# Kernel optimization log

Measured on AMD Instinct MI355X. Metric: run time of the kernel, lower is better.

## Reference

```python
import jax, jax.numpy as jnp
import numpy as np

# graph/batch constants
B, N_PER, DEG, FEAT, K = 64, 1024, 16, 64, 10
N = B * N_PER            # 65536 total nodes
E = N * DEG              # 1048576 edges
HID = 2 * FEAT           # 128


def setup_inputs() -> dict:
    key = jax.random.key(0)
    ks = jax.random.split(key, 10)
    x = jax.random.normal(ks[0], (N, FEAT), jnp.float32)
    # intra-graph edges: local indices in [0, n) offset by graph id * n
    offs = (jnp.arange(B, dtype=jnp.int32) * N_PER)[:, None]
    edge_src = (jax.random.randint(ks[1], (B, N_PER * DEG), 0, N_PER, jnp.int32) + offs).reshape(-1)
    edge_dst = (jax.random.randint(ks[2], (B, N_PER * DEG), 0, N_PER, jnp.int32) + offs).reshape(-1)
    uniforms = jax.random.uniform(ks[3], (N, 3 * K), jnp.float32, 1e-6, 1.0 - 1e-6)

    def lin(k, i, o):
        s = 1.0 / np.sqrt(i)
        return jax.random.uniform(k, (i, o), jnp.float32, -s, s)

    return {
        "x": x, "edge_src": edge_src, "edge_dst": edge_dst, "uniforms": uniforms,
        "W0": lin(ks[4], FEAT, HID), "b0": jnp.zeros((HID,), jnp.float32),
        "W1": lin(ks[5], HID, HID), "b1": jnp.zeros((HID,), jnp.float32),
        "Wf": lin(ks[6], HID, HID), "bf": jnp.zeros((HID,), jnp.float32),
        "W2": lin(ks[7], 2 * HID, HID), "b2": jnp.zeros((HID,), jnp.float32),
        "W3": lin(ks[8], HID, 1), "b3": jnp.zeros((1,), jnp.float32),
    }


def _gcn_norm(src, dst):
    # GCNConv: add self-loops, symmetric deg^{-1/2} normalization
    loop = jnp.arange(N, dtype=src.dtype)
    s = jnp.concatenate([src, loop])
    d = jnp.concatenate([dst, loop])
    deg = jnp.zeros((N,), jnp.float32).at[d].add(1.0)
    dinv = jax.lax.rsqrt(deg)  # deg >= 1 because of self-loops
    return s, d, dinv[s] * dinv[d]


def _gcn(h, W, b, s, d, norm):
    h = h @ W                                                   # [N, out]
    agg = jnp.zeros((N, W.shape[1]), h.dtype).at[d].add(h[s] * norm[:, None])
    return agg + b


def reference(x, edge_src, edge_dst, uniforms, W0, b0, W1, b1, Wf, bf, W2, b2, W3, b3):
    s, d, norm = _gcn_norm(edge_src, edge_dst)
    # conv0 + global max pool + fc1 -> per-graph global info
    h0 = jax.nn.relu(_gcn(x, W0, b0, s, d, norm))               # [N, HID]
    glob = jnp.max(h0.reshape(B, N_PER, HID), axis=1) @ Wf + bf  # [B, HID]
    # two applications of the SAME conv1 (as in the source)
    h = jax.nn.relu(_gcn(h0, W1, b1, s, d, norm))
    h = jax.nn.relu(_gcn(h, W1, b1, s, d, norm))
    # ConcatenateLayer: [local, tiled global] per node (dropout is eval identity)
    h = jnp.concatenate([h, jnp.repeat(glob, N_PER, axis=0)], axis=-1)  # [N, 2*HID]
    h = jax.nn.relu(_gcn(h, W2, b2, s, d, norm))
    logits = _gcn(h, W3, b3, s, d, norm).reshape(B, N_PER)      # [B, n]
    # SampleConcrete (eval): per-graph top-k threshold mask
    th = jax.lax.top_k(logits, K)[0][:, -1]                     # kth-largest per graph
    mask = (logits >= th[:, None]).astype(jnp.float32)
    return mask.reshape(N, 1)
```

## Files before the change

kernel.cpp:

```cpp
#include <hip/hip_runtime.h>
#include <math.h>

#define NB    64
#define NPER  1024
#define NTOT  65536
#define ETOT  1048576
#define FEAT  64
#define HID   128
#define KSEL  10
#define MAXDEG 64


typedef __attribute__((ext_vector_type(8))) short bf16x8;
typedef __attribute__((ext_vector_type(4))) float f32x4;

static __device__ __forceinline__ unsigned short f2bf(float x) {
    unsigned u = __float_as_uint(x);
    return (unsigned short)((u + 0x7FFFu + ((u >> 16) & 1u)) >> 16);
}
static __device__ __forceinline__ float bf2f(unsigned short s) {
    return __uint_as_float(((unsigned)s) << 16);
}

__global__ __launch_bounds__(1024) void csrpack_k(const int* __restrict__ src,
                                                  const int* __restrict__ dst,
                                                  int* __restrict__ cnt,
                                                  unsigned short* __restrict__ col16,
                                                  const float* __restrict__ W0,
                                                  const float* __restrict__ W1,
                                                  const float* __restrict__ W2,
                                                  unsigned short* __restrict__ Wph,
                                                  unsigned short* __restrict__ Wpl,
                                                  float* __restrict__ part) {
    int t = threadIdx.x;
    int b = blockIdx.x;
    if (b >= NB) {
        int pb = b - NB;
        if (pb == 40) {
            for (int i = t; i < NB * 128; i += 1024) part[i] = 0.f;
            return;
        }
        int idx = pb * 1024 + t;
        if (idx >= 320 * 128) return;
        int k = idx >> 7;
        int c = idx & 127;
        float v;
        size_t mb;
        int kk;
        if (k < 64)       { kk = k;       v = W0[kk * 128 + c]; mb = 0; }
        else if (k < 192) { kk = k - 64;  v = W1[kk * 128 + c]; mb = (size_t)64 * 128; }
        else              { kk = k - 192; v = W2[kk * 128 + c]; mb = (size_t)192 * 128; }
        unsigned short h  = f2bf(v);
        unsigned short lo = f2bf(v - bf2f(h));
        size_t d = mb + ((size_t)(kk >> 3) * 128 + c) * 8 + (kk & 7);
        Wph[d] = h;
        Wpl[d] = lo;
        return;
    }
    __shared__ int lcnt[NPER];
    int g = b;
    int gbase = g << 10;
    int ebase = g * (NPER * 16);
    lcnt[t] = 0;
    __syncthreads();
    const int4* ds4 = (const int4*)(dst + ebase);
    const int4* ss4 = (const int4*)(src + ebase);
#pragma unroll 1
    for (int i = 0; i < 4; ++i) {
        int e4 = i * 1024 + t;
        int4 dv = ds4[e4];
        int4 sv = ss4[e4];
        int d0 = dv.x & (NPER - 1), s0 = sv.x & (NPER - 1);
        int d1 = dv.y & (NPER - 1), s1 = sv.y & (NPER - 1);
        int d2 = dv.z & (NPER - 1), s2 = sv.z & (NPER - 1);
        int d3 = dv.w & (NPER - 1), s3 = sv.w & (NPER - 1);
        int p0 = atomicAdd(&lcnt[d0], 1);
        col16[(size_t)(gbase + d0) * MAXDEG + p0] = (unsigned short)s0;
        int p1 = atomicAdd(&lcnt[d1], 1);
        col16[(size_t)(gbase + d1) * MAXDEG + p1] = (unsigned short)s1;
        int p2 = atomicAdd(&lcnt[d2], 1);
        col16[(size_t)(gbase + d2) * MAXDEG + p2] = (unsigned short)s2;
        int p3 = atomicAdd(&lcnt[d3], 1);
        col16[(size_t)(gbase + d3) * MAXDEG + p3] = (unsigned short)s3;
    }
    __syncthreads();
    cnt[gbase + t] = lcnt[t];
}

__global__ __launch_bounds__(1024) void agg_k(const float* __restrict__ Z,
                                              const float* __restrict__ x,
                                              const unsigned short* __restrict__ col16,
                                              const int* __restrict__ cnt,
                                              unsigned short* __restrict__ Ah,
                                              unsigned short* __restrict__ Al,
                                              int cshift,
                                              float* __restrict__ fvec,
                                              const float* __restrict__ Wf,
                                              const float* __restrict__ bfv,
                                              const float* __restrict__ W2g,
                                              float* __restrict__ gproj,
                                              const float* __restrict__ part) {
    __shared__ float4 sy4[4096];
    int t = threadIdx.x;

    if (Wf && (int)blockIdx.x >= (int)gridDim.x - NB) {
        float* sm = (float*)sy4;
        float* mp = sm;
        float* ps = sm + 128;
        float* gl = sm + 128 + 1024;
        int gg = blockIdx.x - (gridDim.x - NB);
        int o = t & 127, s8 = t >> 7;
        if (t < 128) mp[t] = part[(size_t)gg * 128 + t];
        __syncthreads();
        float p = 0.f;
#pragma unroll
        for (int q = 0; q < 16; ++q) { int k = s8 * 16 + q; p += mp[k] * Wf[(size_t)k * 128 + o]; }
        ps[t] = p;
        __syncthreads();
        if (t < 128) {
            float a = bfv[t];
#pragma unroll
            for (int q = 0; q < 8; ++q) a += ps[q * 128 + t];
            gl[t] = a;
        }
        __syncthreads();
        p = 0.f;
#pragma unroll
        for (int q = 0; q < 16; ++q) { int k = s8 * 16 + q; p += gl[k] * W2g[(size_t)(128 + k) * 128 + o]; }
        ps[t] = p;
        __syncthreads();
        if (t < 128) {
            float a = 0.f;
#pragma unroll
            for (int q = 0; q < 8; ++q) a += ps[q * 128 + t];
            gproj[(size_t)gg * 128 + t] = a;
        }
        return;
    }

    int g = blockIdx.x >> cshift;
    int c = blockIdx.x & ((1 << cshift) - 1);
    int gbase = g << 10;

    if (x) {
#pragma unroll
        for (int j = 0; j < 4; ++j) {
            int fl = j * 1024 + t;
            int v = fl >> 2, q = fl & 3;
            float dvv = rsqrtf((float)cnt[gbase + v] + 1.0f);
            float4 z = *(const float4*)&x[(size_t)(gbase + v) * FEAT + c * 16 + q * 4];
            z.x *= dvv; z.y *= dvv; z.z *= dvv; z.w *= dvv;
            sy4[fl] = z;
        }
    } else {
        const float4* Zg4 = (const float4*)(Z + ((size_t)c * NTOT + gbase) * 16);
#pragma unroll
        for (int j = 0; j < 4; ++j) sy4[j * 1024 + t] = Zg4[j * 1024 + t];
    }
    __syncthreads();

    int f4 = t & 3;
    int vl = t >> 2;

#pragma unroll 1
    for (int pass = 0; pass < 4; ++pass) {
        int v = pass * 256 + vl;
        int gv = gbase + v;
        int n = cnt[gv];
        float dv = rsqrtf((float)n + 1.0f);
        const unsigned short* ip = col16 + (size_t)gv * MAXDEG;
        float4 acc = sy4[v * 4 + f4];
        int i = 0;
        for (; i + 4 <= n; i += 4) {
            ushort4 s4 = *(const ushort4*)&ip[i];
            float4 y0 = sy4[(int)s4.x * 4 + f4];
            float4 y1 = sy4[(int)s4.y * 4 + f4];
            float4 y2 = sy4[(int)s4.z * 4 + f4];
            float4 y3 = sy4[(int)s4.w * 4 + f4];
            acc.x += (y0.x + y1.x) + (y2.x + y3.x);
            acc.y += (y0.y + y1.y) + (y2.y + y3.y);
            acc.z += (y0.z + y1.z) + (y2.z + y3.z);
            acc.w += (y0.w + y1.w) + (y2.w + y3.w);
        }
        for (; i < n; ++i) {
            float4 ya = sy4[(int)ip[i] * 4 + f4];
            acc.x += ya.x; acc.y += ya.y; acc.z += ya.z; acc.w += ya.w;
        }
        acc.x *= dv; acc.y *= dv; acc.z *= dv; acc.w *= dv;
        int krow = c * 16 + f4 * 4;
        size_t ba = ((size_t)(krow >> 3) * NTOT + gv) * 8 + (krow & 7);
        ushort4 h, lo;
        h.x = f2bf(acc.x); lo.x = f2bf(acc.x - bf2f(h.x));
        h.y = f2bf(acc.y); lo.y = f2bf(acc.y - bf2f(h.y));
        h.z = f2bf(acc.z); lo.z = f2bf(acc.z - bf2f(h.z));
        h.w = f2bf(acc.w); lo.w = f2bf(acc.w - bf2f(h.w));
        *(ushort4*)&Ah[ba] = h;
        *(ushort4*)&Al[ba] = lo;
    }

    if (fvec && c == 0) {
        __syncthreads();
        float* sdv = (float*)sy4;
        float dv = rsqrtf((float)cnt[gbase + t] + 1.0f);
        sdv[t] = dv;
        __syncthreads();
        int n = cnt[gbase + t];
        float acc = dv;
        const unsigned short* ip = col16 + (size_t)(gbase + t) * MAXDEG;
        int i = 0;
        for (; i + 4 <= n; i += 4) {
            ushort4 s4 = *(const ushort4*)&ip[i];
            acc += (sdv[s4.x] + sdv[s4.y]) + (sdv[s4.z] + sdv[s4.w]);
        }
        for (; i < n; ++i) acc += sdv[ip[i]];
        fvec[gbase + t] = dv * acc;
    }
}

__global__ __launch_bounds__(256, 4) void gemm_k(const unsigned short* __restrict__ Ah,
                                                 const unsigned short* __restrict__ Al,
                                                 const unsigned short* __restrict__ Wph,
                                                 const unsigned short* __restrict__ Wpl,
                                                 const float* __restrict__ bias,
                                                 float* __restrict__ outZ,
                                                 int K,
                                                 const float* __restrict__ fvec,
                                                 const float* __restrict__ gproj,
                                                 float* __restrict__ part,
                                                 const float* __restrict__ W3,
                                                 const int* __restrict__ cnt,
                                                 float* __restrict__ zout) {
    __shared__ __align__(16) unsigned short sAh[64 * 128];
    __shared__ __align__(16) unsigned short sAl[64 * 128];
    __shared__ float zred[4 * 64];

    int t = threadIdx.x;
    int row0 = blockIdx.x * 64;
    int w = t >> 6;
    int l = t & 63;
    int lr = l & 15;
    int hg = l >> 4;

    f32x4 acc[4][2];
#pragma unroll
    for (int m = 0; m < 4; ++m)
#pragma unroll
        for (int n = 0; n < 2; ++n) acc[m][n] = (f32x4){0.f, 0.f, 0.f, 0.f};

    int nu = (K >> 3) << 6 >> 8;
    for (int i = 0; i < nu; ++i) {
        int u = t + i * 256;
        int p = u >> 6, r = u & 63;
        size_t src = ((size_t)p * NTOT + row0 + r) * 8;
        *(uint4*)&sAh[u * 8] = *(const uint4*)&Ah[src];
        *(uint4*)&sAl[u * 8] = *(const uint4*)&Al[src];
    }
    __syncthreads();

    int nk = K >> 5;
#pragma unroll 1
    for (int s = 0; s < nk; ++s) {
        int pb = s * 4 + hg;
        bf16x8 ah[4], al[4], bh[2], bl[2];
#pragma unroll
        for (int m = 0; m < 4; ++m) {
            ah[m] = *(const bf16x8*)&sAh[(pb * 64 + m * 16 + lr) * 8];
            al[m] = *(const bf16x8*)&sAl[(pb * 64 + m * 16 + lr) * 8];
        }
#pragma unroll
        for (int n = 0; n < 2; ++n) {
            size_t wb = ((size_t)pb * 128 + w * 32 + n * 16 + lr) * 8;
            bh[n] = *(const bf16x8*)&Wph[wb];
            bl[n] = *(const bf16x8*)&Wpl[wb];
        }
#pragma unroll
        for (int m = 0; m < 4; ++m)
#pragma unroll
            for (int n = 0; n < 2; ++n) {
                acc[m][n] = __builtin_amdgcn_mfma_f32_16x16x32_bf16(ah[m], bh[n], acc[m][n], 0, 0, 0);
                acc[m][n] = __builtin_amdgcn_mfma_f32_16x16x32_bf16(al[m], bh[n], acc[m][n], 0, 0, 0);
                acc[m][n] = __builtin_amdgcn_mfma_f32_16x16x32_bf16(ah[m], bl[n], acc[m][n], 0, 0, 0);
            }
    }

    int g = row0 >> 10;
    int wc0 = w * 32;
    float bb[2], gp[2], w3c[2];
#pragma unroll
    for (int n = 0; n < 2; ++n) {
        int col = wc0 + n * 16 + lr;
        bb[n]  = bias[col];
        gp[n]  = fvec ? gproj[(size_t)g * 128 + col] : 0.f;
        w3c[n] = zout ? W3[col] : 0.f;
    }
    float fr[4][4];
    if (fvec) {
#pragma unroll
        for (int m = 0; m < 4; ++m)
#pragma unroll
            for (int r = 0; r < 4; ++r) fr[m][r] = fvec[row0 + m * 16 + hg * 4 + r];
    }
    float dvs[4][4];
    if (outZ) {
#pragma unroll
        for (int m = 0; m < 4; ++m)
#pragma unroll
            for (int r = 0; r < 4; ++r)
                dvs[m][r] = rsqrtf((float)cnt[row0 + m * 16 + hg * 4 + r] + 1.0f);
    }
    float zp[4][4];
#pragma unroll
    for (int m = 0; m < 4; ++m)
#pragma unroll
        for (int r = 0; r < 4; ++r) zp[m][r] = 0.f;
    float cmx[2] = {0.f, 0.f};

#pragma unroll
    for (int m = 0; m < 4; ++m)
#pragma unroll
        for (int n = 0; n < 2; ++n)
#pragma unroll
            for (int r = 0; r < 4; ++r) {
                float v = acc[m][n][r] + bb[n];
                if (fvec) v += fr[m][r] * gp[n];
                v = fmaxf(v, 0.f);
                if (part) cmx[n] = fmaxf(cmx[n], v);
                if (zout) zp[m][r] += v * w3c[n];
                if (outZ) {
                    int row = row0 + m * 16 + hg * 4 + r;
                    int cidx = w * 2 + n;
                    outZ[((size_t)cidx * NTOT + row) * 16 + lr] = v * dvs[m][r];
                }
            }

    if (part) {
#pragma unroll
        for (int n = 0; n < 2; ++n) {
            float v = cmx[n];
            v = fmaxf(v, __shfl_xor(v, 16));
            v = fmaxf(v, __shfl_xor(v, 32));
            if (hg == 0)
                atomicMax((int*)&part[(size_t)g * 128 + wc0 + n * 16 + lr],
                          __float_as_int(v));
        }
    }

    if (zout) {
#pragma unroll
        for (int m = 0; m < 4; ++m)
#pragma unroll
            for (int r = 0; r < 4; ++r) {
                float v = zp[m][r];
                v += __shfl_xor(v, 1);
                v += __shfl_xor(v, 2);
                v += __shfl_xor(v, 4);
                v += __shfl_xor(v, 8);
                zp[m][r] = v;
            }
        if (lr == 0) {
#pragma unroll
            for (int m = 0; m < 4; ++m)
#pragma unroll
                for (int r = 0; r < 4; ++r)
                    zred[w * 64 + m * 16 + hg * 4 + r] = zp[m][r];
        }
        __syncthreads();
        if (t < 64) {
            float sZ = zred[t] + zred[64 + t] + zred[128 + t] + zred[192 + t];
            zout[row0 + t] = sZ * rsqrtf((float)cnt[row0 + t] + 1.0f);
        }
    }
}

__global__ __launch_bounds__(1024) void smask_k(const float* __restrict__ z,
                                                const unsigned short* __restrict__ col16,
                                                const int* __restrict__ cnt,
                                                const float* __restrict__ b3,
                                                float* __restrict__ out) {
    __shared__ float sz[1024];
    __shared__ float sl[1024];
    __shared__ float slo[1024];
    __shared__ float rv[16];
    __shared__ int   ri[16];
    __shared__ float sth;
    int g = blockIdx.x, t = threadIdx.x;
    int wv = t >> 6, ln = t & 63;
    int base = g << 10;
    sz[t] = z[base + t];
    __syncthreads();
    float bb = b3[0];
    {
        int gv = base + t;
        int n = cnt[gv];
        float dv = rsqrtf((float)n + 1.0f);
        float acc = sz[t];
        const unsigned short* ip = col16 + (size_t)gv * MAXDEG;
        int j = 0;
        for (; j + 4 <= n; j += 4) {
            ushort4 s4 = *(const ushort4*)&ip[j];
            acc += (sz[s4.x] + sz[s4.y]) + (sz[s4.z] + sz[s4.w]);
        }
        for (; j < n; ++j) acc += sz[ip[j]];
        float lg = acc * dv + bb;
        sl[t] = lg; slo[t] = lg;
    }
    __syncthreads();
    for (int pass = 0; pass < KSEL; ++pass) {
        float bv = sl[t];
        int bi = t;
#pragma unroll
        for (int off = 32; off; off >>= 1) {
            float ov = __shfl_xor(bv, off);
            int   oi = __shfl_xor(bi, off);
            if (ov > bv || (ov == bv && oi < bi)) { bv = ov; bi = oi; }
        }
        if (ln == 0) { rv[wv] = bv; ri[wv] = bi; }
        __syncthreads();
        if (t == 0) {
            float mv = rv[0]; int mi = ri[0];
#pragma unroll
            for (int q = 1; q < 16; ++q)
                if (rv[q] > mv || (rv[q] == mv && ri[q] < mi)) { mv = rv[q]; mi = ri[q]; }
            sth = mv; sl[mi] = -INFINITY;
        }
        __syncthreads();
    }
    float th = sth;
    out[base + t] = (slo[t] >= th) ? 1.f : 0.f;
}

extern "C" void kernel_launch(void* const* d_in, const int* in_sizes, int n_in,
                              void* d_out, int out_size, void* d_ws, size_t ws_size,
                              hipStream_t stream) {
    const float* x        = (const float*)d_in[0];
    const int*   edge_src = (const int*)d_in[1];
    const int*   edge_dst = (const int*)d_in[2];
    const float* W0 = (const float*)d_in[4];
    const float* b0 = (const float*)d_in[5];
    const float* W1 = (const float*)d_in[6];
    const float* b1 = (const float*)d_in[7];
    const float* Wf = (const float*)d_in[8];
    const float* bf = (const float*)d_in[9];
    const float* W2 = (const float*)d_in[10];
    const float* b2 = (const float*)d_in[11];
    const float* W3 = (const float*)d_in[12];
    const float* b3 = (const float*)d_in[13];
    float* out = (float*)d_out;

    char* w = (char*)d_ws;
    int*            cnt   = (int*)w;            w += (size_t)NTOT * 4;
    unsigned short* col16 = (unsigned short*)w; w += (size_t)NTOT * MAXDEG * 2;
    float*          fvec  = (float*)w;          w += (size_t)NTOT * 4;
    unsigned short* Ah    = (unsigned short*)w; w += (size_t)NTOT * 128 * 2;
    unsigned short* Al    = (unsigned short*)w; w += (size_t)NTOT * 128 * 2;
    float*          Q     = (float*)w;          w += (size_t)NTOT * 128 * 4;
    float*          part  = (float*)w;          w += (size_t)NB * 128 * 4;
    float*          gproj = (float*)w;          w += (size_t)NB * 128 * 4;
    float*          z     = (float*)w;          w += (size_t)NTOT * 4;
    unsigned short* Wph   = (unsigned short*)w; w += (size_t)320 * 128 * 2;
    unsigned short* Wpl   = (unsigned short*)w; w += (size_t)320 * 128 * 2;

    csrpack_k<<<NB + 41, 1024, 0, stream>>>(edge_src, edge_dst, cnt, col16,
                                            W0, W1, W2, Wph, Wpl, part);

    agg_k<<<NB * 4, 1024, 0, stream>>>(nullptr, x, col16, cnt, Ah, Al, 2, nullptr,
                                       nullptr, nullptr, nullptr, nullptr, nullptr);
    gemm_k<<<NTOT / 64, 256, 0, stream>>>(Ah, Al, Wph, Wpl, b0, Q, FEAT,
                                          nullptr, nullptr, part, nullptr, cnt, nullptr);

    agg_k<<<NB * 8 + NB, 1024, 0, stream>>>(Q, nullptr, col16, cnt, Ah, Al, 3, nullptr,
                                            Wf, bf, W2, gproj, part);
    gemm_k<<<NTOT / 64, 256, 0, stream>>>(Ah, Al, Wph + 64 * 128, Wpl + 64 * 128, b1, Q,
                                          HID, nullptr, nullptr, nullptr, nullptr, cnt,
                                          nullptr);
    agg_k<<<NB * 8, 1024, 0, stream>>>(Q, nullptr, col16, cnt, Ah, Al, 3, nullptr,
                                       nullptr, nullptr, nullptr, nullptr, nullptr);
    gemm_k<<<NTOT / 64, 256, 0, stream>>>(Ah, Al, Wph + 64 * 128, Wpl + 64 * 128, b1, Q,
                                          HID, nullptr, nullptr, nullptr, nullptr, cnt,
                                          nullptr);

    agg_k<<<NB * 8, 1024, 0, stream>>>(Q, nullptr, col16, cnt, Ah, Al, 3, fvec,
                                       nullptr, nullptr, nullptr, nullptr, nullptr);
    gemm_k<<<NTOT / 64, 256, 0, stream>>>(Ah, Al, Wph + 192 * 128, Wpl + 192 * 128, b2,
                                          nullptr, HID, fvec, gproj, nullptr, W3, cnt, z);

    smask_k<<<NB, 1024, 0, stream>>>(z, col16, cnt, b3, out);
}
```

Measured before the change: 299.4 us.

## Transpose CSR neighbor lists and map one node per thread in aggregation

Neighbor indices are now stored slot-major (slot * NTOT + node), so consecutive threads read consecutive nodes' k-th neighbor and the index loads coalesce. The aggregation kernel switches from four threads per node over four passes to one thread per node covering all 16 features, so each index is loaded once instead of four times. A swizzled shared-memory layout (SQ) is added to reduce LDS bank conflicts for the per-node float4 gathers. In exchange each thread holds more registers, and per-thread loop lengths vary with node degree, which can cause divergence within a wavefront.

Measured after the change: 326.2 us. 9.0% more time.

```diff
diff --git a/kernel.cpp b/kernel.cpp
--- a/kernel.cpp
+++ b/kernel.cpp
@@ -13,6 +13,8 @@
 
 typedef __attribute__((ext_vector_type(8))) short bf16x8;
 typedef __attribute__((ext_vector_type(4))) float f32x4;
+
+#define SQ(v, q) (((v) << 2) + ((q) ^ ((v) & 3)))
 
 static __device__ __forceinline__ unsigned short f2bf(float x) {
     unsigned u = __float_as_uint(x);
@@ -75,13 +77,13 @@
         int d2 = dv.z & (NPER - 1), s2 = sv.z & (NPER - 1);
         int d3 = dv.w & (NPER - 1), s3 = sv.w & (NPER - 1);
         int p0 = atomicAdd(&lcnt[d0], 1);
-        col16[(size_t)(gbase + d0) * MAXDEG + p0] = (unsigned short)s0;
+        col16[(size_t)p0 * NTOT + gbase + d0] = (unsigned short)s0;
         int p1 = atomicAdd(&lcnt[d1], 1);
-        col16[(size_t)(gbase + d1) * MAXDEG + p1] = (unsigned short)s1;
+        col16[(size_t)p1 * NTOT + gbase + d1] = (unsigned short)s1;
         int p2 = atomicAdd(&lcnt[d2], 1);
-        col16[(size_t)(gbase + d2) * MAXDEG + p2] = (unsigned short)s2;
+        col16[(size_t)p2 * NTOT + gbase + d2] = (unsigned short)s2;
         int p3 = atomicAdd(&lcnt[d3], 1);
-        col16[(size_t)(gbase + d3) * MAXDEG + p3] = (unsigned short)s3;
+        col16[(size_t)p3 * NTOT + gbase + d3] = (unsigned short)s3;
     }
     __syncthreads();
     cnt[gbase + t] = lcnt[t];
@@ -150,70 +152,102 @@
             float dvv = rsqrtf((float)cnt[gbase + v] + 1.0f);
             float4 z = *(const float4*)&x[(size_t)(gbase + v) * FEAT + c * 16 + q * 4];
             z.x *= dvv; z.y *= dvv; z.z *= dvv; z.w *= dvv;
-            sy4[fl] = z;
+            sy4[SQ(v, q)] = z;
         }
     } else {
         const float4* Zg4 = (const float4*)(Z + ((size_t)c * NTOT + gbase) * 16);
 #pragma unroll
-        for (int j = 0; j < 4; ++j) sy4[j * 1024 + t] = Zg4[j * 1024 + t];
+        for (int j = 0; j < 4; ++j) {
+            int fl = j * 1024 + t;
+            int v = fl >> 2, q = fl & 3;
+            sy4[SQ(v, q)] = Zg4[fl];
+        }
     }
     __syncthreads();
 
-    int f4 = t & 3;
-    int vl = t >> 2;
-
-#pragma unroll 1
-    for (int pass = 0; pass < 4; ++pass) {
-        int v = pass * 256 + vl;
-        int gv = gbase + v;
-        int n = cnt[gv];
-        float dv = rsqrtf((float)n + 1.0f);
-        const unsigned short* ip = col16 + (size_t)gv * MAXDEG;
-        float4 acc = sy4[v * 4 + f4];
-        int i = 0;
-        for (; i + 4 <= n; i += 4) {
-            ushort4 s4 = *(const ushort4*)&ip[i];
-            float4 y0 = sy4[(int)s4.x * 4 + f4];
-            float4 y1 = sy4[(int)s4.y * 4 + f4];
-            float4 y2 = sy4[(int)s4.z * 4 + f4];
-            float4 y3 = sy4[(int)s4.w * 4 + f4];
-            acc.x += (y0.x + y1.x) + (y2.x + y3.x);
-            acc.y += (y0.y + y1.y) + (y2.y + y3.y);
-            acc.z += (y0.z + y1.z) + (y2.z + y3.z);
-            acc.w += (y0.w + y1.w) + (y2.w + y3.w);
-        }
-        for (; i < n; ++i) {
-            float4 ya = sy4[(int)ip[i] * 4 + f4];
-            acc.x += ya.x; acc.y += ya.y; acc.z += ya.z; acc.w += ya.w;
-        }
-        acc.x *= dv; acc.y *= dv; acc.z *= dv; acc.w *= dv;
-        int krow = c * 16 + f4 * 4;
-        size_t ba = ((size_t)(krow >> 3) * NTOT + gv) * 8 + (krow & 7);
+    int v = t;
+    int gv = gbase + v;
+    int n = cnt[gv];
+    float dv = rsqrtf((float)n + 1.0f);
+    const unsigned short* ip = col16 + gv;
+    float4 a0 = sy4[SQ(v, 0)];
+    float4 a1 = sy4[SQ(v, 1)];
+    float4 a2 = sy4[SQ(v, 2)];
+    float4 a3 = sy4[SQ(v, 3)];
+    int i = 0;
+    for (; i + 2 <= n; i += 2) {
+        int pa = ip[(size_t)i * NTOT];
+        int pb = ip[(size_t)(i + 1) * NTOT];
+        float4 ya0 = sy4[SQ(pa, 0)];
+        float4 ya1 = sy4[SQ(pa, 1)];
+        float4 ya2 = sy4[SQ(pa, 2)];
+        float4 ya3 = sy4[SQ(pa, 3)];
+        float4 yb0 = sy4[SQ(pb, 0)];
+        float4 yb1 = sy4[SQ(pb, 1)];
+        float4 yb2 = sy4[SQ(pb, 2)];
+        float4 yb3 = sy4[SQ(pb, 3)];
+        a0.x += ya0.x + yb0.x; a0.y += ya0.y + yb0.y; a0.z += ya0.z + yb0.z; a0.w += ya0.w + yb0.w;
+        a1.x += ya1.x + yb1.x; a1.y += ya1.y + yb1.y; a1.z += ya1.z + yb1.z; a1.w += ya1.w + yb1.w;
+        a2.x += ya2.x + yb2.x; a2.y += ya2.y + yb2.y; a2.z += ya2.z + yb2.z; a2.w += ya2.w + yb2.w;
+        a3.x += ya3.x + yb3.x; a3.y += ya3.y + yb3.y; a3.z += ya3.z + yb3.z; a3.w += ya3.w + yb3.w;
+    }
+    if (i < n) {
+        int pa = ip[(size_t)i * NTOT];
+        float4 ya0 = sy4[SQ(pa, 0)];
+        float4 ya1 = sy4[SQ(pa, 1)];
+        float4 ya2 = sy4[SQ(pa, 2)];
+        float4 ya3 = sy4[SQ(pa, 3)];
+        a0.x += ya0.x; a0.y += ya0.y; a0.z += ya0.z; a0.w += ya0.w;
+        a1.x += ya1.x; a1.y += ya1.y; a1.z += ya1.z; a1.w += ya1.w;
+        a2.x += ya2.x; a2.y += ya2.y; a2.z += ya2.z; a2.w += ya2.w;
+        a3.x += ya3.x; a3.y += ya3.y; a3.z += ya3.z; a3.w += ya3.w;
+    }
+    a0.x *= dv; a0.y *= dv; a0.z *= dv; a0.w *= dv;
+    a1.x *= dv; a1.y *= dv; a1.z *= dv; a1.w *= dv;
+    a2.x *= dv; a2.y *= dv; a2.z *= dv; a2.w *= dv;
+    a3.x *= dv; a3.y *= dv; a3.z *= dv; a3.w *= dv;
+
+    {
         ushort4 h, lo;
-        h.x = f2bf(acc.x); lo.x = f2bf(acc.x - bf2f(h.x));
-        h.y = f2bf(acc.y); lo.y = f2bf(acc.y - bf2f(h.y));
-        h.z = f2bf(acc.z); lo.z = f2bf(acc.z - bf2f(h.z));
-        h.w = f2bf(acc.w); lo.w = f2bf(acc.w - bf2f(h.w));
+        size_t ba = ((size_t)(2 * c) * NTOT + gv) * 8;
+        h.x = f2bf(a0.x); lo.x = f2bf(a0.x - bf2f(h.x));
+        h.y = f2bf(a0.y); lo.y = f2bf(a0.y - bf2f(h.y));
+        h.z = f2bf(a0.z); lo.z = f2bf(a0.z - bf2f(h.z));
+        h.w = f2bf(a0.w); lo.w = f2bf(a0.w - bf2f(h.w));
         *(ushort4*)&Ah[ba] = h;
         *(ushort4*)&Al[ba] = lo;
+        h.x = f2bf(a1.x); lo.x = f2bf(a1.x - bf2f(h.x));
+        h.y = f2bf(a1.y); lo.y = f2bf(a1.y - bf2f(h.y));
+        h.z = f2bf(a1.z); lo.z = f2bf(a1.z - bf2f(h.z));
+        h.w = f2bf(a1.w); lo.w = f2bf(a1.w - bf2f(h.w));
+        *(ushort4*)&Ah[ba + 4] = h;
+        *(ushort4*)&Al[ba + 4] = lo;
+        size_t bb = ((size_t)(2 * c + 1) * NTOT + gv) * 8;
+        h.x = f2bf(a2.x); lo.x = f2bf(a2.x - bf2f(h.x));
+        h.y = f2bf(a2.y); lo.y = f2bf(a2.y - bf2f(h.y));
+        h.z = f2bf(a2.z); lo.z = f2bf(a2.z - bf2f(h.z));
+        h.w = f2bf(a2.w); lo.w = f2bf(a2.w - bf2f(h.w));
+        *(ushort4*)&Ah[bb] = h;
+        *(ushort4*)&Al[bb] = lo;
+        h.x = f2bf(a3.x); lo.x = f2bf(a3.x - bf2f(h.x));
+        h.y = f2bf(a3.y); lo.y = f2bf(a3.y - bf2f(h.y));
+        h.z = f2bf(a3.z); lo.z = f2bf(a3.z - bf2f(h.z));
+        h.w = f2bf(a3.w); lo.w = f2bf(a3.w - bf2f(h.w));
+        *(ushort4*)&Ah[bb + 4] = h;
+        *(ushort4*)&Al[bb + 4] = lo;
     }
 
     if (fvec && c == 0) {
         __syncthreads();
         float* sdv = (float*)sy4;
-        float dv = rsqrtf((float)cnt[gbase + t] + 1.0f);
-        sdv[t] = dv;
-        __syncthreads();
-        int n = cnt[gbase + t];
-        float acc = dv;
-        const unsigned short* ip = col16 + (size_t)(gbase + t) * MAXDEG;
-        int i = 0;
-        for (; i + 4 <= n; i += 4) {
-            ushort4 s4 = *(const ushort4*)&ip[i];
-            acc += (sdv[s4.x] + sdv[s4.y]) + (sdv[s4.z] + sdv[s4.w]);
-        }
-        for (; i < n; ++i) acc += sdv[ip[i]];
-        fvec[gbase + t] = dv * acc;
+        float dvv = rsqrtf((float)cnt[gbase + t] + 1.0f);
+        sdv[t] = dvv;
+        __syncthreads();
+        int nn = cnt[gbase + t];
+        float acc = dvv;
+        const unsigned short* ipf = col16 + gbase + t;
+        for (int j = 0; j < nn; ++j) acc += sdv[ipf[(size_t)j * NTOT]];
+        fvec[gbase + t] = dvv * acc;
     }
 }
 
@@ -394,13 +428,11 @@
         int n = cnt[gv];
         float dv = rsqrtf((float)n + 1.0f);
         float acc = sz[t];
-        const unsigned short* ip = col16 + (size_t)gv * MAXDEG;
+        const unsigned short* ip = col16 + gv;
         int j = 0;
-        for (; j + 4 <= n; j += 4) {
-            ushort4 s4 = *(const ushort4*)&ip[j];
-            acc += (sz[s4.x] + sz[s4.y]) + (sz[s4.z] + sz[s4.w]);
-        }
-        for (; j < n; ++j) acc += sz[ip[j]];
+        for (; j + 2 <= n; j += 2)
+            acc += sz[ip[(size_t)j * NTOT]] + sz[ip[(size_t)(j + 1) * NTOT]];
+        for (; j < n; ++j) acc += sz[ip[(size_t)j * NTOT]];
         float lg = acc * dv + bb;
         sl[t] = lg; slo[t] = lg;
     }
```
